# Performance work log

Hardware: AMD Instinct MI355X
Metric: run time of the kernel (lower is better)

Reference implementation:

```python
import jax, jax.numpy as jnp
import numpy as np

N_NODES = 100000
N_EDGES = 3200000  # avg degree 32
D_IN = 128
D_OUT = 64


def setup_inputs() -> dict:
    key = jax.random.key(0)
    k1, k2, k3, k4, k5 = jax.random.split(key, 5)
    h = jax.random.normal(k1, (N_NODES, D_IN), dtype=jnp.float32)
    W = jax.random.normal(k2, (D_IN, D_OUT), dtype=jnp.float32) / np.float32(np.sqrt(D_IN))
    a = jax.random.normal(k3, (2 * D_OUT,), dtype=jnp.float32) / np.float32(np.sqrt(2 * D_OUT))
    src = jax.random.randint(k4, (N_EDGES,), 0, N_NODES, dtype=jnp.int32)
    dst = jax.random.randint(k5, (N_EDGES,), 0, N_NODES, dtype=jnp.int32)
    return {"h": h, "W": W, "a": a, "src": src, "dst": dst}


def reference(h, W, a, src, dst):
    N = h.shape[0]
    d = W.shape[1]
    # node projection: z = linear(h)  (bias-free, n_mlp_layer=1)
    z = h @ W  # [N, d]
    # edge attention logit: attn_linear(cat([z_src, z_dst])) == z_src@a[:d] + z_dst@a[d:]
    e = z[src] @ a[:d] + z[dst] @ a[d:]  # [E]
    # segment softmax over incoming edges of each destination node
    m = jax.ops.segment_max(e, dst, num_segments=N)  # [N]
    w = jnp.exp(e - m[dst])  # [E]
    s = jax.ops.segment_sum(w, dst, num_segments=N)  # [N]
    alpha = w / s[dst]  # [E]
    # weighted scatter-sum of source features (nodes with no in-edges stay 0, as in DGL)
    out = jax.ops.segment_sum(alpha[:, None] * z[src], dst, num_segments=N)  # [N, d]
    return out
```

## Files before the change

### kernel.cpp

```cpp
#include <hip/hip_runtime.h>

#define D_IN 128
#define D_OUT 64
#define SCAN_ITEMS 2048
#define TILE 8192
#define BSHIFT 7
#define NBK 128
#define MAXNB 1024
#define CAP 8192
#define BN 64
#define HS_STRIDE 132
#define MAXSB 1024

typedef float f32x4 __attribute__((ext_vector_type(4)));
typedef int   i32x4 __attribute__((ext_vector_type(4)));

__device__ __forceinline__ unsigned short f32_to_bf16(float f) {
    unsigned int u = __float_as_uint(f);
    u += 0x7fffu + ((u >> 16) & 1u);
    return (unsigned short)(u >> 16);
}

__global__ __launch_bounds__(256) void k_project(
    const float* __restrict__ h, const float* __restrict__ W,
    const float* __restrict__ a, unsigned short* __restrict__ z16,
    float* __restrict__ E, int n_nodes)
{
    __shared__ float ws[D_IN * D_OUT];
    __shared__ float hs[BN * HS_STRIDE];

    const int tid = threadIdx.x;
    const int nbase = blockIdx.x * BN;

#pragma unroll
    for (int i = 0; i < 8; ++i) {
        int f = (tid + 256 * i) * 4;
        *(float4*)&ws[f] = *(const float4*)&W[f];
    }
#pragma unroll
    for (int j = 0; j < 8; ++j) {
        int f = tid + 256 * j;
        int row = f >> 5;
        int kk = (f & 31) << 2;
        int gr = nbase + row;
        float4 v = make_float4(0.f, 0.f, 0.f, 0.f);
        if (gr < n_nodes) v = *(const float4*)&h[(size_t)gr * D_IN + kk];
        *(float4*)&hs[row * HS_STRIDE + kk] = v;
    }
    __syncthreads();

    const int c4 = (tid & 15) * 4;
    const int n4 = (tid >> 4) * 4;

    float acc[4][4];
#pragma unroll
    for (int i = 0; i < 4; ++i)
#pragma unroll
        for (int j = 0; j < 4; ++j) acc[i][j] = 0.0f;

    for (int k = 0; k < D_IN; k += 4) {
        float4 wv0 = *(float4*)&ws[(k + 0) * D_OUT + c4];
        float4 wv1 = *(float4*)&ws[(k + 1) * D_OUT + c4];
        float4 wv2 = *(float4*)&ws[(k + 2) * D_OUT + c4];
        float4 wv3 = *(float4*)&ws[(k + 3) * D_OUT + c4];
#pragma unroll
        for (int i = 0; i < 4; ++i) {
            float4 hv = *(float4*)&hs[(n4 + i) * HS_STRIDE + k];
            acc[i][0] = fmaf(hv.x, wv0.x, acc[i][0]);
            acc[i][1] = fmaf(hv.x, wv0.y, acc[i][1]);
            acc[i][2] = fmaf(hv.x, wv0.z, acc[i][2]);
            acc[i][3] = fmaf(hv.x, wv0.w, acc[i][3]);
            acc[i][0] = fmaf(hv.y, wv1.x, acc[i][0]);
            acc[i][1] = fmaf(hv.y, wv1.y, acc[i][1]);
            acc[i][2] = fmaf(hv.y, wv1.z, acc[i][2]);
            acc[i][3] = fmaf(hv.y, wv1.w, acc[i][3]);
            acc[i][0] = fmaf(hv.z, wv2.x, acc[i][0]);
            acc[i][1] = fmaf(hv.z, wv2.y, acc[i][1]);
            acc[i][2] = fmaf(hv.z, wv2.z, acc[i][2]);
            acc[i][3] = fmaf(hv.z, wv2.w, acc[i][3]);
            acc[i][0] = fmaf(hv.w, wv3.x, acc[i][0]);
            acc[i][1] = fmaf(hv.w, wv3.y, acc[i][1]);
            acc[i][2] = fmaf(hv.w, wv3.z, acc[i][2]);
            acc[i][3] = fmaf(hv.w, wv3.w, acc[i][3]);
        }
    }

    float a0 = a[c4 + 0], a1 = a[c4 + 1], a2 = a[c4 + 2], a3 = a[c4 + 3];
#pragma unroll
    for (int i = 0; i < 4; ++i) {
        int node = nbase + n4 + i;
        bool ok = node < n_nodes;
        if (ok) {
            ushort4 q;
            q.x = f32_to_bf16(acc[i][0]);
            q.y = f32_to_bf16(acc[i][1]);
            q.z = f32_to_bf16(acc[i][2]);
            q.w = f32_to_bf16(acc[i][3]);
            *(ushort4*)&z16[(size_t)node * D_OUT + c4] = q;
        }
        float es_p = acc[i][0] * a0 + acc[i][1] * a1 + acc[i][2] * a2 + acc[i][3] * a3;
        es_p += __shfl_xor(es_p, 1, 64);
        es_p += __shfl_xor(es_p, 2, 64);
        es_p += __shfl_xor(es_p, 4, 64);
        es_p += __shfl_xor(es_p, 8, 64);
        if ((tid & 15) == 0 && ok)
            E[node] = __expf(fminf(fmaxf(es_p, -60.0f), 60.0f));
    }
}

__global__ __launch_bounds__(512) void k_hist2(
    const int* __restrict__ dst, unsigned int* __restrict__ btot,
    int n_edges, int NB)
{
    __shared__ unsigned int hcnt[MAXNB];
    int t = blockIdx.x;
    for (int b = threadIdx.x; b < NB; b += 512) hcnt[b] = 0;
    __syncthreads();
    int base = t * TILE;
    int lim = min(base + TILE, n_edges);
    for (int i = base + threadIdx.x * 4; i < lim; i += 2048) {
        if (i + 4 <= lim) {
            i32x4 d4 = __builtin_nontemporal_load((const i32x4*)&dst[i]);
            atomicAdd(&hcnt[(unsigned int)d4.x >> BSHIFT], 1u);
            atomicAdd(&hcnt[(unsigned int)d4.y >> BSHIFT], 1u);
            atomicAdd(&hcnt[(unsigned int)d4.z >> BSHIFT], 1u);
            atomicAdd(&hcnt[(unsigned int)d4.w >> BSHIFT], 1u);
        } else {
            for (int k = i; k < lim; ++k)
                atomicAdd(&hcnt[(unsigned int)dst[k] >> BSHIFT], 1u);
        }
    }
    __syncthreads();
    for (int b = threadIdx.x; b < NB; b += 512) {
        unsigned int c = hcnt[b];
        if (c) atomicAdd(&btot[b], c);
    }
}

__global__ __launch_bounds__(256) void k_bscan(
    const unsigned int* __restrict__ btot, unsigned int* __restrict__ boff,
    unsigned int* __restrict__ gcur, int nb)
{
    __shared__ unsigned int tmp[256];
    int tid = threadIdx.x;
    unsigned int v[8]; unsigned int tsum = 0;
#pragma unroll
    for (int j = 0; j < 8; ++j) {
        int idx = tid * 8 + j;
        v[j] = (idx < nb) ? btot[idx] : 0u;
        tsum += v[j];
    }
    tmp[tid] = tsum; __syncthreads();
    for (int o = 1; o < 256; o <<= 1) {
        unsigned int u = (tid >= o) ? tmp[tid - o] : 0u; __syncthreads();
        tmp[tid] += u; __syncthreads();
    }
    unsigned int run = tmp[tid] - tsum;
#pragma unroll
    for (int j = 0; j < 8; ++j) {
        int idx = tid * 8 + j;
        if (idx < nb) { boff[idx] = run; gcur[idx] = run; }
        run += v[j];
    }
    if (tid == 255) boff[nb] = tmp[255];
}

__global__ __launch_bounds__(512) void k_partition2(
    const int* __restrict__ src, const int* __restrict__ dst,
    unsigned int* __restrict__ gcur, unsigned int* __restrict__ tmp,
    int n_edges, int NB)
{
    __shared__ unsigned int cnt[MAXNB];
    const int t = blockIdx.x;
    const int tid = threadIdx.x;
    const int base = t * TILE;
    const int lim = min(base + TILE, n_edges);

    for (int b = tid; b < NB; b += 512) cnt[b] = 0;
    __syncthreads();

    unsigned int dv[16], sv[16];
#pragma unroll
    for (int j = 0; j < 4; ++j) {
        int i = base + tid * 4 + j * 2048;
        if (i + 4 <= lim) {
            i32x4 d4 = __builtin_nontemporal_load((const i32x4*)&dst[i]);
            i32x4 s4 = __builtin_nontemporal_load((const i32x4*)&src[i]);
            dv[4 * j + 0] = (unsigned int)d4.x; sv[4 * j + 0] = (unsigned int)s4.x;
            dv[4 * j + 1] = (unsigned int)d4.y; sv[4 * j + 1] = (unsigned int)s4.y;
            dv[4 * j + 2] = (unsigned int)d4.z; sv[4 * j + 2] = (unsigned int)s4.z;
            dv[4 * j + 3] = (unsigned int)d4.w; sv[4 * j + 3] = (unsigned int)s4.w;
        } else {
#pragma unroll
            for (int k = 0; k < 4; ++k) {
                int ii = i + k;
                bool ok = ii < lim;
                dv[4 * j + k] = ok ? (unsigned int)dst[ii] : 0xFFFFFFFFu;
                sv[4 * j + k] = ok ? (unsigned int)src[ii] : 0u;
            }
        }
    }

#pragma unroll
    for (int k = 0; k < 16; ++k) {
        unsigned int d = dv[k];
        if (d != 0xFFFFFFFFu) atomicAdd(&cnt[d >> BSHIFT], 1u);
    }
    __syncthreads();

    for (int b = tid; b < NB; b += 512) {
        unsigned int c = cnt[b];
        cnt[b] = c ? atomicAdd(&gcur[b], c) : 0u;
    }
    __syncthreads();

#pragma unroll
    for (int k = 0; k < 16; ++k) {
        unsigned int d = dv[k];
        if (d != 0xFFFFFFFFu) {
            unsigned int pos = atomicAdd(&cnt[d >> BSHIFT], 1u);
            tmp[pos] = (sv[k] << BSHIFT) | (d & (NBK - 1u));
        }
    }
}

__global__ __launch_bounds__(512) void k_gather(
    const unsigned int* __restrict__ tmp, const unsigned int* __restrict__ boff,
    const float* __restrict__ E, const unsigned short* __restrict__ z16,
    int* __restrict__ sscratch, float* __restrict__ out,
    int n_edges, int n_nodes, int NB)
{
    __shared__ unsigned int offL[NBK + 1];
    __shared__ unsigned int cnt[NBK];
    __shared__ unsigned int sedge[CAP];

    const int b = blockIdx.x;
    const int tid = threadIdx.x;
    const unsigned int s0 = boff[b];
    const unsigned int s1 = boff[b + 1];
    const unsigned int sz = s1 - s0;
    const bool inLds = (sz <= CAP);

    unsigned int ev[16];
    if (inLds) {
#pragma unroll
        for (int j = 0; j < 16; ++j) {
            unsigned int i = s0 + (unsigned int)tid + 512u * (unsigned int)j;
            ev[j] = (i < s1) ? __builtin_nontemporal_load(&tmp[i]) : 0u;
        }
    }

    if (tid < NBK) cnt[tid] = 0;
    __syncthreads();
    if (inLds) {
#pragma unroll
        for (int j = 0; j < 16; ++j) {
            unsigned int i = s0 + (unsigned int)tid + 512u * (unsigned int)j;
            if (i < s1) atomicAdd(&cnt[ev[j] & (NBK - 1u)], 1u);
        }
    } else {
        for (unsigned int i = s0 + tid; i < s1; i += 512)
            atomicAdd(&cnt[tmp[i] & (NBK - 1u)], 1u);
    }
    __syncthreads();

    if (tid < 64) {
        unsigned int c0 = cnt[2 * tid], c1 = cnt[2 * tid + 1];
        unsigned int ps = c0 + c1;
        unsigned int run = ps;
#pragma unroll
        for (int o = 1; o < 64; o <<= 1) {
            unsigned int u = __shfl_up(run, o, 64);
            if (tid >= o) run += u;
        }
        unsigned int excl = run - ps;
        offL[2 * tid]     = excl;
        offL[2 * tid + 1] = excl + c0;
        cnt[2 * tid]      = excl;
        cnt[2 * tid + 1]  = excl + c0;
        if (tid == 63) offL[NBK] = run;
    }
    __syncthreads();

    if (inLds) {
#pragma unroll
        for (int j = 0; j < 16; ++j) {
            unsigned int i = s0 + (unsigned int)tid + 512u * (unsigned int)j;
            if (i < s1) {
                unsigned int val = ev[j];
                unsigned int pos = atomicAdd(&cnt[val & (NBK - 1u)], 1u);
                sedge[pos] = val >> BSHIFT;
            }
        }
    } else {
        for (unsigned int i = s0 + tid; i < s1; i += 512) {
            unsigned int val = tmp[i];
            unsigned int pos = atomicAdd(&cnt[val & (NBK - 1u)], 1u);
            sscratch[s0 + pos] = (int)(val >> BSHIFT);
        }
    }
    __syncthreads();

    const int wave = tid >> 6;
    const int lane = tid & 63;
    const int g = lane >> 3;
    const int fl = lane & 7;

    for (int dl = wave; dl < NBK; dl += 8) {
        int node = (b << BSHIFT) + dl;
        if (node >= n_nodes) break;
        unsigned int a0 = offL[dl], a1 = offL[dl + 1];
        float* orow = out + (size_t)node * D_OUT;
        if (a0 == a1) {
            if (g == 0) {
                __builtin_nontemporal_store((f32x4)0.f, (f32x4*)(orow + fl * 8));
                __builtin_nontemporal_store((f32x4)0.f, (f32x4*)(orow + fl * 8 + 4));
            }
            continue;
        }

        float acc[8];
#pragma unroll
        for (int j = 0; j < 8; ++j) acc[j] = 0.0f;
        float wsum = 0.0f;

        unsigned int i = a0 + (unsigned int)g;
        if (inLds) {
            for (; i + 8 < a1; i += 16) {
                int sn0 = (int)sedge[i];
                int sn1 = (int)sedge[i + 8];
                float w0 = E[sn0];
                float w1 = E[sn1];
                uint4 p0 = *(const uint4*)(z16 + (size_t)sn0 * D_OUT + fl * 8);
                uint4 p1 = *(const uint4*)(z16 + (size_t)sn1 * D_OUT + fl * 8);
                wsum += w0 + w1;
                const unsigned int pu0[4] = {p0.x, p0.y, p0.z, p0.w};
                const unsigned int pu1[4] = {p1.x, p1.y, p1.z, p1.w};
#pragma unroll
                for (int q = 0; q < 4; ++q) {
                    acc[2 * q]     = fmaf(w0, __uint_as_float(pu0[q] << 16),         acc[2 * q]);
                    acc[2 * q + 1] = fmaf(w0, __uint_as_float(pu0[q] & 0xffff0000u), acc[2 * q + 1]);
                    acc[2 * q]     = fmaf(w1, __uint_as_float(pu1[q] << 16),         acc[2 * q]);
                    acc[2 * q + 1] = fmaf(w1, __uint_as_float(pu1[q] & 0xffff0000u), acc[2 * q + 1]);
                }
            }
            if (i < a1) {
                int sn = (int)sedge[i];
                float w = E[sn];
                const uint4 p = *(const uint4*)(z16 + (size_t)sn * D_OUT + fl * 8);
                wsum += w;
                const unsigned int pu[4] = {p.x, p.y, p.z, p.w};
#pragma unroll
                for (int q = 0; q < 4; ++q) {
                    acc[2 * q]     = fmaf(w, __uint_as_float(pu[q] << 16),         acc[2 * q]);
                    acc[2 * q + 1] = fmaf(w, __uint_as_float(pu[q] & 0xffff0000u), acc[2 * q + 1]);
                }
            }
        } else {
            for (; i < a1; i += 8) {
                int sn = sscratch[s0 + i];
                float w = E[sn];
                const uint4 p = *(const uint4*)(z16 + (size_t)sn * D_OUT + fl * 8);
                wsum += w;
                const unsigned int pu[4] = {p.x, p.y, p.z, p.w};
#pragma unroll
                for (int q = 0; q < 4; ++q) {
                    acc[2 * q]     = fmaf(w, __uint_as_float(pu[q] << 16),         acc[2 * q]);
                    acc[2 * q + 1] = fmaf(w, __uint_as_float(pu[q] & 0xffff0000u), acc[2 * q + 1]);
                }
            }
        }

#pragma unroll
        for (int o = 8; o <= 32; o <<= 1) {
#pragma unroll
            for (int j = 0; j < 8; ++j) acc[j] += __shfl_xor(acc[j], o, 64);
            wsum += __shfl_xor(wsum, o, 64);
        }

        if (g == 0) {
            float inv = __builtin_amdgcn_rcpf(wsum);
            f32x4 o0 = {acc[0] * inv, acc[1] * inv, acc[2] * inv, acc[3] * inv};
            f32x4 o1 = {acc[4] * inv, acc[5] * inv, acc[6] * inv, acc[7] * inv};
            __builtin_nontemporal_store(o0, (f32x4*)(orow + fl * 8));
            __builtin_nontemporal_store(o1, (f32x4*)(orow + fl * 8 + 4));
        }
    }
}

__global__ __launch_bounds__(256) void k_rank(
    const int* __restrict__ dst, unsigned int* __restrict__ count,
    unsigned short* __restrict__ rank, int n_edges)
{
    int e = blockIdx.x * blockDim.x + threadIdx.x;
    if (e < n_edges) rank[e] = (unsigned short)atomicAdd(&count[dst[e]], 1u);
}

__global__ __launch_bounds__(256) void k_place(
    const int* __restrict__ src, const int* __restrict__ dst,
    const unsigned int* __restrict__ off, const unsigned short* __restrict__ rank,
    int* __restrict__ ssrc, int n_edges)
{
    int e = blockIdx.x * blockDim.x + threadIdx.x;
    if (e < n_edges) ssrc[off[dst[e]] + (unsigned int)rank[e]] = src[e];
}

__global__ __launch_bounds__(256) void k_count(
    const int* __restrict__ dst, unsigned int* __restrict__ count, int n_edges)
{
    int e = blockIdx.x * blockDim.x + threadIdx.x;
    if (e < n_edges) atomicAdd(&count[dst[e]], 1u);
}

__global__ __launch_bounds__(256) void k_fill(
    const int* __restrict__ src, const int* __restrict__ dst,
    unsigned int* __restrict__ cursor, int* __restrict__ ssrc, int n_edges)
{
    int e = blockIdx.x * blockDim.x + threadIdx.x;
    if (e < n_edges) {
        unsigned int pos = atomicAdd(&cursor[dst[e]], 1u);
        ssrc[pos] = src[e];
    }
}

__global__ __launch_bounds__(256) void k_fused(
    const int* __restrict__ ssrc, const unsigned int* __restrict__ off,
    const float* __restrict__ E, const unsigned short* __restrict__ z16,
    float* __restrict__ out, int n_nodes)
{
    int node = (blockIdx.x * blockDim.x + threadIdx.x) >> 6;
    int lane = threadIdx.x & 63;
    if (node >= n_nodes) return;
    int g  = lane >> 3;
    int fl = lane & 7;

    unsigned int start = off[node], end = off[node + 1];
    float* orow = out + (size_t)node * D_OUT;
    if (start == end) {
        if (g == 0) {
            *(float4*)(orow + fl * 8)     = make_float4(0.f, 0.f, 0.f, 0.f);
            *(float4*)(orow + fl * 8 + 4) = make_float4(0.f, 0.f, 0.f, 0.f);
        }
        return;
    }

    float acc[8];
#pragma unroll
    for (int j = 0; j < 8; ++j) acc[j] = 0.0f;
    float wsum = 0.0f;

    for (unsigned int i = start + g; i < end; i += 8) {
        int sn = ssrc[i];
        float w = E[sn];
        wsum += w;
        const uint4 p = *(const uint4*)(z16 + (size_t)sn * D_OUT + fl * 8);
        const unsigned int pu[4] = {p.x, p.y, p.z, p.w};
#pragma unroll
        for (int q = 0; q < 4; ++q) {
            float lo = __uint_as_float(pu[q] << 16);
            float hi = __uint_as_float(pu[q] & 0xffff0000u);
            acc[2 * q]     = fmaf(w, lo, acc[2 * q]);
            acc[2 * q + 1] = fmaf(w, hi, acc[2 * q + 1]);
        }
    }

#pragma unroll
    for (int o = 8; o <= 32; o <<= 1) {
#pragma unroll
        for (int j = 0; j < 8; ++j) acc[j] += __shfl_xor(acc[j], o, 64);
        wsum += __shfl_xor(wsum, o, 64);
    }

    if (g == 0) {
        float inv = 1.0f / wsum;
        float4 o0 = make_float4(acc[0] * inv, acc[1] * inv, acc[2] * inv, acc[3] * inv);
        float4 o1 = make_float4(acc[4] * inv, acc[5] * inv, acc[6] * inv, acc[7] * inv);
        *(float4*)(orow + fl * 8)     = o0;
        *(float4*)(orow + fl * 8 + 4) = o1;
    }
}

__global__ __launch_bounds__(256) void k_scan1(
    const unsigned int* __restrict__ count, unsigned int* __restrict__ off,
    unsigned int* __restrict__ blk_sums, int n)
{
    __shared__ unsigned int tmp[256];
    int tid = threadIdx.x;
    int base = blockIdx.x * SCAN_ITEMS;
    unsigned int v[8]; unsigned int tsum = 0;
#pragma unroll
    for (int i = 0; i < 8; ++i) {
        int idx = base + tid * 8 + i;
        v[i] = (idx < n) ? count[idx] : 0u;
        tsum += v[i];
    }
    tmp[tid] = tsum; __syncthreads();
    for (int o = 1; o < 256; o <<= 1) {
        unsigned int u = (tid >= o) ? tmp[tid - o] : 0u; __syncthreads();
        tmp[tid] += u; __syncthreads();
    }
    unsigned int run = tmp[tid] - tsum;
    if (tid == 255) blk_sums[blockIdx.x] = tmp[255];
#pragma unroll
    for (int i = 0; i < 8; ++i) {
        int idx = base + tid * 8 + i;
        if (idx < n) off[idx] = run;
        run += v[i];
    }
}

__global__ __launch_bounds__(256) void k_scan2(
    const unsigned int* __restrict__ blk_sums, unsigned int* __restrict__ blk_offs,
    unsigned int* __restrict__ off, int nblocks, int n)
{
    __shared__ unsigned int tmp[256];
    int tid = threadIdx.x;
    unsigned int carry = 0;
    for (int base = 0; base < nblocks; base += 256) {
        unsigned int v = (base + tid < nblocks) ? blk_sums[base + tid] : 0u;
        tmp[tid] = v; __syncthreads();
        for (int o = 1; o < 256; o <<= 1) {
            unsigned int u = (tid >= o) ? tmp[tid - o] : 0u; __syncthreads();
            tmp[tid] += u; __syncthreads();
        }
        if (base + tid < nblocks) blk_offs[base + tid] = carry + tmp[tid] - v;
        carry += tmp[255];
        __syncthreads();
    }
    if (tid == 0) off[n] = carry;
}

__global__ __launch_bounds__(256) void k_scan3(
    unsigned int* __restrict__ off, unsigned int* __restrict__ cursor,
    const unsigned int* __restrict__ blk_offs, int n)
{
    int i = blockIdx.x * blockDim.x + threadIdx.x;
    if (i < n) {
        unsigned int o = off[i] + blk_offs[i / SCAN_ITEMS];
        off[i] = o; cursor[i] = o;
    }
}

extern "C" void kernel_launch(void* const* d_in, const int* in_sizes, int n_in,
                              void* d_out, int out_size, void* d_ws, size_t ws_size,
                              hipStream_t stream) {
    const float* h   = (const float*)d_in[0];
    const float* W   = (const float*)d_in[1];
    const float* a   = (const float*)d_in[2];
    const int*   src = (const int*)d_in[3];
    const int*   dst = (const int*)d_in[4];
    float* out = (float*)d_out;

    const int n_nodes = in_sizes[0] / D_IN;
    const int n_edges = in_sizes[3];

    const int NB = (n_nodes + NBK - 1) >> BSHIFT;
    const int NT = (n_edges + TILE - 1) / TILE;

    auto align = [](size_t x) { return (x + 255) & ~(size_t)255; };
    char* w = (char*)d_ws;
    unsigned short* z16 = (unsigned short*)w;  w += align((size_t)n_nodes * D_OUT * sizeof(unsigned short));
    float* E = (float*)w;                      w += align((size_t)n_nodes * sizeof(float));
    unsigned int* off = (unsigned int*)w;      w += align(((size_t)n_nodes + 1) * sizeof(unsigned int));
    unsigned int* blk_sums = (unsigned int*)w; w += align(MAXSB * sizeof(unsigned int));
    unsigned int* blk_offs = (unsigned int*)w; w += align(MAXSB * sizeof(unsigned int));
    size_t hist_elems = (size_t)n_nodes > 8192 ? (size_t)n_nodes : (size_t)8192;
    unsigned int* histT = (unsigned int*)w;    w += align(hist_elems * sizeof(unsigned int));
    unsigned int* btot = histT;
    unsigned int* boff = histT + 2048;
    unsigned int* gcur = histT + 4352;
    unsigned int* count = histT;
    int* ssrc = (int*)w;                       w += align((size_t)n_edges * sizeof(int));
    unsigned int* tmp = (unsigned int*)w;
    unsigned short* rank = (unsigned short*)tmp;
    size_t need_sort = ((char*)tmp - (char*)d_ws) + align((size_t)n_edges * sizeof(unsigned int));
    size_t need_rank = ((char*)tmp - (char*)d_ws) + align((size_t)n_edges * sizeof(unsigned short));

    const bool use_sort = (ws_size >= need_sort) && NB <= MAXNB &&
                          n_nodes < (1 << 25);
    const bool use_rank = !use_sort && (ws_size >= need_rank);

    k_project<<<(n_nodes + BN - 1) / BN, 256, 0, stream>>>(h, W, a, z16, E, n_nodes);

    const int eblocks = (n_edges + 255) / 256;
    const int sb_node = (n_nodes + SCAN_ITEMS - 1) / SCAN_ITEMS;

    if (use_sort) {
        hipMemsetAsync(btot, 0, (size_t)(NB + 1) * sizeof(unsigned int), stream);
        k_hist2<<<NT, 512, 0, stream>>>(dst, btot, n_edges, NB);
        k_bscan<<<1, 256, 0, stream>>>(btot, boff, gcur, NB);
        k_partition2<<<NT, 512, 0, stream>>>(src, dst, gcur, tmp, n_edges, NB);
        k_gather<<<NB, 512, 0, stream>>>(tmp, boff, E, z16, ssrc, out,
                                         n_edges, n_nodes, NB);
    } else if (use_rank) {
        hipMemsetAsync(count, 0, (size_t)n_nodes * sizeof(unsigned int), stream);
        k_rank<<<eblocks, 256, 0, stream>>>(dst, count, rank, n_edges);
        k_scan1<<<sb_node, 256, 0, stream>>>(count, off, blk_sums, n_nodes);
        k_scan2<<<1, 256, 0, stream>>>(blk_sums, blk_offs, off, sb_node, n_nodes);
        k_scan3<<<(n_nodes + 255) / 256, 256, 0, stream>>>(off, count, blk_offs, n_nodes);
        k_place<<<eblocks, 256, 0, stream>>>(src, dst, off, rank, ssrc, n_edges);
        k_fused<<<(n_nodes + 3) / 4, 256, 0, stream>>>(ssrc, off, E, z16, out, n_nodes);
    } else {
        hipMemsetAsync(count, 0, (size_t)n_nodes * sizeof(unsigned int), stream);
        k_count<<<eblocks, 256, 0, stream>>>(dst, count, n_edges);
        k_scan1<<<sb_node, 256, 0, stream>>>(count, off, blk_sums, n_nodes);
        k_scan2<<<1, 256, 0, stream>>>(blk_sums, blk_offs, off, sb_node, n_nodes);
        k_scan3<<<(n_nodes + 255) / 256, 256, 0, stream>>>(off, count, blk_offs, n_nodes);
        k_fill<<<eblocks, 256, 0, stream>>>(src, dst, count, ssrc, n_edges);
        k_fused<<<(n_nodes + 3) / 4, 256, 0, stream>>>(ssrc, off, E, z16, out, n_nodes);
    }
}
```

Measured before the change: 246.7 us.

## Fuse node projection into partition kernel as extra blocks with 512 threads

The projection kernel is folded into the edge-partition launch: the first NPT blocks do the partition pass and the remaining blocks compute z and the exponentiated source logits. The projection now uses 512 threads per block with two nodes per thread instead of four. The aim is to save one launch and let the compute-bound projection overlap with the memory-bound partition pass. The cost is that the partition blocks now request the projection's large LDS allocation, which can lower their occupancy.

```diff
diff --git a/kernel.cpp b/kernel.cpp
--- a/kernel.cpp
+++ b/kernel.cpp
@@ -11,6 +11,7 @@
 #define BN 64
 #define HS_STRIDE 132
 #define MAXSB 1024
+#define PROJ_LDS (D_IN * D_OUT + BN * HS_STRIDE)
 
 typedef float f32x4 __attribute__((ext_vector_type(4)));
 typedef int   i32x4 __attribute__((ext_vector_type(4)));
@@ -21,25 +22,22 @@
     return (unsigned short)(u >> 16);
 }
 
-__global__ __launch_bounds__(256) void k_project(
+__device__ __forceinline__ void proj_body512(
+    float* ws, float* hs,
     const float* __restrict__ h, const float* __restrict__ W,
     const float* __restrict__ a, unsigned short* __restrict__ z16,
-    float* __restrict__ E, int n_nodes)
-{
-    __shared__ float ws[D_IN * D_OUT];
-    __shared__ float hs[BN * HS_STRIDE];
-
-    const int tid = threadIdx.x;
-    const int nbase = blockIdx.x * BN;
-
-#pragma unroll
-    for (int i = 0; i < 8; ++i) {
-        int f = (tid + 256 * i) * 4;
+    float* __restrict__ E, int n_nodes, int blk, int tid)
+{
+    const int nbase = blk * BN;
+
+#pragma unroll
+    for (int i = 0; i < 4; ++i) {
+        int f = (tid + 512 * i) * 4;
         *(float4*)&ws[f] = *(const float4*)&W[f];
     }
 #pragma unroll
-    for (int j = 0; j < 8; ++j) {
-        int f = tid + 256 * j;
+    for (int j = 0; j < 4; ++j) {
+        int f = tid + 512 * j;
         int row = f >> 5;
         int kk = (f & 31) << 2;
         int gr = nbase + row;
@@ -50,11 +48,11 @@
     __syncthreads();
 
     const int c4 = (tid & 15) * 4;
-    const int n4 = (tid >> 4) * 4;
-
-    float acc[4][4];
-#pragma unroll
-    for (int i = 0; i < 4; ++i)
+    const int n2 = (tid >> 4) * 2;
+
+    float acc[2][4];
+#pragma unroll
+    for (int i = 0; i < 2; ++i)
 #pragma unroll
         for (int j = 0; j < 4; ++j) acc[i][j] = 0.0f;
 
@@ -64,8 +62,8 @@
         float4 wv2 = *(float4*)&ws[(k + 2) * D_OUT + c4];
         float4 wv3 = *(float4*)&ws[(k + 3) * D_OUT + c4];
 #pragma unroll
-        for (int i = 0; i < 4; ++i) {
-            float4 hv = *(float4*)&hs[(n4 + i) * HS_STRIDE + k];
+        for (int i = 0; i < 2; ++i) {
+            float4 hv = *(float4*)&hs[(n2 + i) * HS_STRIDE + k];
             acc[i][0] = fmaf(hv.x, wv0.x, acc[i][0]);
             acc[i][1] = fmaf(hv.x, wv0.y, acc[i][1]);
             acc[i][2] = fmaf(hv.x, wv0.z, acc[i][2]);
@@ -87,8 +85,8 @@
 
     float a0 = a[c4 + 0], a1 = a[c4 + 1], a2 = a[c4 + 2], a3 = a[c4 + 3];
 #pragma unroll
-    for (int i = 0; i < 4; ++i) {
-        int node = nbase + n4 + i;
+    for (int i = 0; i < 2; ++i) {
+        int node = nbase + n2 + i;
         bool ok = node < n_nodes;
         if (ok) {
             ushort4 q;
@@ -106,6 +104,16 @@
         if ((tid & 15) == 0 && ok)
             E[node] = __expf(fminf(fmaxf(es_p, -60.0f), 60.0f));
     }
+}
+
+__global__ __launch_bounds__(512) void k_project(
+    const float* __restrict__ h, const float* __restrict__ W,
+    const float* __restrict__ a, unsigned short* __restrict__ z16,
+    float* __restrict__ E, int n_nodes)
+{
+    __shared__ float smem[PROJ_LDS];
+    proj_body512(smem, smem + D_IN * D_OUT, h, W, a, z16, E, n_nodes,
+                 blockIdx.x, threadIdx.x);
 }
 
 __global__ __launch_bounds__(512) void k_hist2(
@@ -165,62 +173,72 @@
     if (tid == 255) boff[nb] = tmp[255];
 }
 
-__global__ __launch_bounds__(512) void k_partition2(
+__global__ __launch_bounds__(512) void k_proj_part(
+    const float* __restrict__ h, const float* __restrict__ W,
+    const float* __restrict__ a, unsigned short* __restrict__ z16,
+    float* __restrict__ E,
     const int* __restrict__ src, const int* __restrict__ dst,
     unsigned int* __restrict__ gcur, unsigned int* __restrict__ tmp,
-    int n_edges, int NB)
-{
-    __shared__ unsigned int cnt[MAXNB];
-    const int t = blockIdx.x;
+    int n_nodes, int n_edges, int NPT, int NB)
+{
+    __shared__ float smem[PROJ_LDS];
     const int tid = threadIdx.x;
-    const int base = t * TILE;
-    const int lim = min(base + TILE, n_edges);
-
-    for (int b = tid; b < NB; b += 512) cnt[b] = 0;
-    __syncthreads();
-
-    unsigned int dv[16], sv[16];
-#pragma unroll
-    for (int j = 0; j < 4; ++j) {
-        int i = base + tid * 4 + j * 2048;
-        if (i + 4 <= lim) {
-            i32x4 d4 = __builtin_nontemporal_load((const i32x4*)&dst[i]);
-            i32x4 s4 = __builtin_nontemporal_load((const i32x4*)&src[i]);
-            dv[4 * j + 0] = (unsigned int)d4.x; sv[4 * j + 0] = (unsigned int)s4.x;
-            dv[4 * j + 1] = (unsigned int)d4.y; sv[4 * j + 1] = (unsigned int)s4.y;
-            dv[4 * j + 2] = (unsigned int)d4.z; sv[4 * j + 2] = (unsigned int)s4.z;
-            dv[4 * j + 3] = (unsigned int)d4.w; sv[4 * j + 3] = (unsigned int)s4.w;
-        } else {
-#pragma unroll
-            for (int k = 0; k < 4; ++k) {
-                int ii = i + k;
-                bool ok = ii < lim;
-                dv[4 * j + k] = ok ? (unsigned int)dst[ii] : 0xFFFFFFFFu;
-                sv[4 * j + k] = ok ? (unsigned int)src[ii] : 0u;
+
+    if ((int)blockIdx.x < NPT) {
+        unsigned int* cnt = (unsigned int*)smem;
+        const int t = blockIdx.x;
+        const int base = t * TILE;
+        const int lim = min(base + TILE, n_edges);
+
+        for (int b = tid; b < NB; b += 512) cnt[b] = 0;
+        __syncthreads();
+
+        unsigned int dv[16], sv[16];
+#pragma unroll
+        for (int j = 0; j < 4; ++j) {
+            int i = base + tid * 4 + j * 2048;
+            if (i + 4 <= lim) {
+                i32x4 d4 = __builtin_nontemporal_load((const i32x4*)&dst[i]);
+                i32x4 s4 = __builtin_nontemporal_load((const i32x4*)&src[i]);
+                dv[4 * j + 0] = (unsigned int)d4.x; sv[4 * j + 0] = (unsigned int)s4.x;
+                dv[4 * j + 1] = (unsigned int)d4.y; sv[4 * j + 1] = (unsigned int)s4.y;
+                dv[4 * j + 2] = (unsigned int)d4.z; sv[4 * j + 2] = (unsigned int)s4.z;
+                dv[4 * j + 3] = (unsigned int)d4.w; sv[4 * j + 3] = (unsigned int)s4.w;
+            } else {
+#pragma unroll
+                for (int k = 0; k < 4; ++k) {
+                    int ii = i + k;
+                    bool ok = ii < lim;
+                    dv[4 * j + k] = ok ? (unsigned int)dst[ii] : 0xFFFFFFFFu;
+                    sv[4 * j + k] = ok ? (unsigned int)src[ii] : 0u;
+                }
             }
         }
-    }
-
-#pragma unroll
-    for (int k = 0; k < 16; ++k) {
-        unsigned int d = dv[k];
-        if (d != 0xFFFFFFFFu) atomicAdd(&cnt[d >> BSHIFT], 1u);
-    }
-    __syncthreads();
-
-    for (int b = tid; b < NB; b += 512) {
-        unsigned int c = cnt[b];
-        cnt[b] = c ? atomicAdd(&gcur[b], c) : 0u;
-    }
-    __syncthreads();
-
-#pragma unroll
-    for (int k = 0; k < 16; ++k) {
-        unsigned int d = dv[k];
-        if (d != 0xFFFFFFFFu) {
-            unsigned int pos = atomicAdd(&cnt[d >> BSHIFT], 1u);
-            tmp[pos] = (sv[k] << BSHIFT) | (d & (NBK - 1u));
-        }
+
+#pragma unroll
+        for (int k = 0; k < 16; ++k) {
+            unsigned int d = dv[k];
+            if (d != 0xFFFFFFFFu) atomicAdd(&cnt[d >> BSHIFT], 1u);
+        }
+        __syncthreads();
+
+        for (int b = tid; b < NB; b += 512) {
+            unsigned int c = cnt[b];
+            cnt[b] = c ? atomicAdd(&gcur[b], c) : 0u;
+        }
+        __syncthreads();
+
+#pragma unroll
+        for (int k = 0; k < 16; ++k) {
+            unsigned int d = dv[k];
+            if (d != 0xFFFFFFFFu) {
+                unsigned int pos = atomicAdd(&cnt[d >> BSHIFT], 1u);
+                tmp[pos] = (sv[k] << BSHIFT) | (d & (NBK - 1u));
+            }
+        }
+    } else {
+        proj_body512(smem, smem + D_IN * D_OUT, h, W, a, z16, E, n_nodes,
+                     blockIdx.x - NPT, tid);
     }
 }
 
@@ -555,7 +573,8 @@
     const int n_edges = in_sizes[3];
 
     const int NB = (n_nodes + NBK - 1) >> BSHIFT;
-    const int NT = (n_edges + TILE - 1) / TILE;
+    const int NPT = (n_edges + TILE - 1) / TILE;
+    const int PB = (n_nodes + BN - 1) / BN;
 
     auto align = [](size_t x) { return (x + 255) & ~(size_t)255; };
     char* w = (char*)d_ws;
@@ -580,19 +599,20 @@
                           n_nodes < (1 << 25);
     const bool use_rank = !use_sort && (ws_size >= need_rank);
 
-    k_project<<<(n_nodes + BN - 1) / BN, 256, 0, stream>>>(h, W, a, z16, E, n_nodes);
-
     const int eblocks = (n_edges + 255) / 256;
     const int sb_node = (n_nodes + SCAN_ITEMS - 1) / SCAN_ITEMS;
 
     if (use_sort) {
         hipMemsetAsync(btot, 0, (size_t)(NB + 1) * sizeof(unsigned int), stream);
-        k_hist2<<<NT, 512, 0, stream>>>(dst, btot, n_edges, NB);
+        k_hist2<<<NPT, 512, 0, stream>>>(dst, btot, n_edges, NB);
         k_bscan<<<1, 256, 0, stream>>>(btot, boff, gcur, NB);
-        k_partition2<<<NT, 512, 0, stream>>>(src, dst, gcur, tmp, n_edges, NB);
+        k_proj_part<<<NPT + PB, 512, 0, stream>>>(h, W, a, z16, E, src, dst,
+                                                  gcur, tmp, n_nodes, n_edges,
+                                                  NPT, NB);
         k_gather<<<NB, 512, 0, stream>>>(tmp, boff, E, z16, ssrc, out,
                                          n_edges, n_nodes, NB);
     } else if (use_rank) {
+        k_project<<<PB, 512, 0, stream>>>(h, W, a, z16, E, n_nodes);
         hipMemsetAsync(count, 0, (size_t)n_nodes * sizeof(unsigned int), stream);
         k_rank<<<eblocks, 256, 0, stream>>>(dst, count, rank, n_edges);
         k_scan1<<<sb_node, 256, 0, stream>>>(count, off, blk_sums, n_nodes);
@@ -601,6 +621,7 @@
         k_place<<<eblocks, 256, 0, stream>>>(src, dst, off, rank, ssrc, n_edges);
         k_fused<<<(n_nodes + 3) / 4, 256, 0, stream>>>(ssrc, off, E, z16, out, n_nodes);
     } else {
+        k_project<<<PB, 512, 0, stream>>>(h, W, a, z16, E, n_nodes);
         hipMemsetAsync(count, 0, (size_t)n_nodes * sizeof(unsigned int), stream);
         k_count<<<eblocks, 256, 0, stream>>>(dst, count, n_edges);
         k_scan1<<<sb_node, 256, 0, stream>>>(count, off, blk_sums, n_nodes);
```

Measured after the change: 236.9 us. -4.0%, faster.
